# Optimization experiments

Measured on AMD Instinct MI355X. Metric: run time of the kernel, lower is better.

The kernel has to match this reference:

```python
import jax, jax.numpy as jnp
import numpy as np

D = 1024
H = 16
DH = D // H
L = 128  # max_pos_len
B = 4
T = 1024
SCALE = float(np.sqrt(D / H))


def setup_inputs() -> dict:
    key = jax.random.key(0)
    ks = jax.random.split(key, 9)
    x_q = jax.random.normal(ks[0], (B, T, D), dtype=jnp.float32)
    x_k = jax.random.normal(ks[1], (B, T, D), dtype=jnp.float32)
    x_v = jax.random.normal(ks[2], (B, T, D), dtype=jnp.float32)
    mask = jax.random.randint(ks[3], (B, 1, 1, T), 0, 2) == 1  # bool, True = masked
    Wq = jax.random.normal(ks[4], (D, D), dtype=jnp.float32) * 0.02
    Wk = jax.random.normal(ks[5], (D, D), dtype=jnp.float32) * 0.02
    Wv = jax.random.normal(ks[6], (D, D), dtype=jnp.float32) * 0.02
    Wo = jax.random.normal(ks[7], (D, D), dtype=jnp.float32) * 0.02
    pos_emb = jax.random.normal(ks[8], (2 * L + 1, DH), dtype=jnp.float32)
    return {"x_q": x_q, "x_k": x_k, "x_v": x_v, "mask": mask,
            "Wq": Wq, "Wk": Wk, "Wv": Wv, "Wo": Wo, "pos_emb": pos_emb}


def reference(x_q, x_k, x_v, mask, Wq, Wk, Wv, Wo, pos_emb):
    # nn.Linear(bias=False): y = x @ W.T
    def split_heads(x):  # (B,T,D) -> (B,H,T,DH)
        return x.reshape(B, -1, H, DH).transpose(0, 2, 1, 3)

    Q = split_heads(x_q @ Wq.T)
    K = split_heads(x_k @ Wk.T)
    V = split_heads(x_v @ Wv.T)

    logits = jnp.einsum('bhqd,bhkd->bhqk', Q, K)

    # arrange_char_pos_embedding: indices[q,k] = clamp(k-q, -L, L) + L
    rel = jnp.clip(jnp.arange(T)[None, :] - jnp.arange(T)[:, None], -L, L) + L
    arranged_pos = pos_emb[rel]  # (T_Q, T_K, DH)
    pos_logits = jnp.einsum('bhqd,qkd->bhqk', Q, arranged_pos)

    logits = (logits + pos_logits) / SCALE
    logits = jnp.where(mask, -jnp.inf, logits)  # mask broadcasts (B,1,1,T)
    attn = jax.nn.softmax(logits, axis=-1)  # dropout p=0.0 -> identity

    combined = jnp.einsum('bhqk,bhkd->bhqd', attn, V)
    heads_concat = combined.transpose(0, 2, 1, 3).reshape(B, -1, D)
    return heads_concat @ Wo.T
```

## Files before the change

kernel.cpp:

```cpp
#include <hip/hip_runtime.h>
#include <hip/hip_bf16.h>
#include <stdint.h>

typedef __attribute__((ext_vector_type(8))) short short8;
typedef __attribute__((ext_vector_type(4))) float f32x4;

__device__ __forceinline__ uint16_t f2bf(float f) {
    union { float f; uint32_t u; } v; v.f = f;
    uint32_t r = v.u + 0x7FFF + ((v.u >> 16) & 1);
    return (uint16_t)(r >> 16);
}
__device__ __forceinline__ float bf2f(uint16_t u) {
    union { uint32_t u; float f; } v; v.u = ((uint32_t)u) << 16;
    return v.f;
}
__device__ __forceinline__ float exp2_raw(float x) {
    float r;
    asm("v_exp_f32 %0, %1" : "=v"(r) : "v"(x));
    return r;
}
__device__ __forceinline__ uint32_t cvt_pk_bf16(float lo, float hi) {
    uint32_t r;
    asm("v_cvt_pk_bf16_f32 %0, %1, %2" : "=v"(r) : "v"(lo), "v"(hi));
    return r;
}

template<int F32>
__device__ __forceinline__ uint4 load8(const void* p, size_t off) {
    if (F32) {
        const float* f = (const float*)p + off;
        float4 f0 = *(const float4*)f;
        float4 f1 = *(const float4*)(f + 4);
        uint4 r;
        r.x = (uint32_t)f2bf(f0.x) | ((uint32_t)f2bf(f0.y) << 16);
        r.y = (uint32_t)f2bf(f0.z) | ((uint32_t)f2bf(f0.w) << 16);
        r.z = (uint32_t)f2bf(f1.x) | ((uint32_t)f2bf(f1.y) << 16);
        r.w = (uint32_t)f2bf(f1.z) | ((uint32_t)f2bf(f1.w) << 16);
        return r;
    } else {
        return *(const uint4*)((const uint16_t*)p + off);
    }
}

#define GLDS(gp, lp) __builtin_amdgcn_global_load_lds( \
    (const __attribute__((address_space(1))) void*)(gp), \
    (__attribute__((address_space(3))) void*)(lp), 16, 0, 0)

struct CvtSeg { const float* s; uint16_t* d; int n8; };
struct CvtArgs { CvtSeg seg[9]; int nseg; const void* mraw; unsigned long long* mbits; };

__global__ __launch_bounds__(256) void cvt_bf16(CvtArgs a)
{
    if (blockIdx.x == 0) {
        __shared__ int flags[3];
        __shared__ uint8_t mloc[4096];
        const uint32_t* w = (const uint32_t*)a.mraw;
        const uint8_t* b8 = (const uint8_t*)a.mraw;
        const int t = threadIdx.x;
        if (t < 3) flags[t] = 0;
        __syncthreads();
        int fbyte = 0, ff32 = 0, fodd = 0;
        for (int i = t; i < 1024; i += 256) {
            uint32_t v = w[i];
            if (v != 0u && v != 1u && v != 0x3F800000u) fbyte = 1;
            if (v == 0x3F800000u) ff32 = 1;
            if ((i & 1) && v != 0u) fodd = 1;
        }
        if (fbyte) atomicOr(&flags[0], 1);
        if (ff32)  atomicOr(&flags[1], 1);
        if (fodd)  atomicOr(&flags[2], 1);
        __syncthreads();
        int mode;
        if (flags[0]) mode = 1;
        else if (flags[1]) mode = 0;
        else if (!flags[2]) mode = 2;
        else mode = 0;
        for (int k = t; k < 4096; k += 256) {
            int val;
            if (mode == 1)      val = (b8[k] != 0);
            else if (mode == 2) val = (w[2 * k] != 0u);
            else                val = (w[k] != 0u);
            mloc[k] = (uint8_t)val;
        }
        __syncthreads();
        if (t < 64) {
            uint64_t bits = 0;
#pragma unroll
            for (int i = 0; i < 64; ++i)
                bits |= (uint64_t)mloc[t * 64 + i] << i;
            a.mbits[t] = bits;
        }
    }
    const int tid = blockIdx.x * 256 + threadIdx.x;
    const int stride = gridDim.x * 256;
    for (int s = 0; s < a.nseg; ++s) {
        const float* src = a.seg[s].s;
        uint16_t* dst = a.seg[s].d;
        const int n8 = a.seg[s].n8;
        if (src) {
            for (int i = tid; i < n8; i += stride)
                *(uint4*)(dst + (size_t)i * 8) = load8<1>(src, (size_t)i * 8);
        } else {
            const uint4 z = {0u, 0u, 0u, 0u};
            for (int i = tid; i < n8; i += stride)
                *(uint4*)(dst + (size_t)i * 8) = z;
        }
    }
}

__global__ __launch_bounds__(256) void gemm128_qkv(
    const uint16_t* __restrict__ xq, const uint16_t* __restrict__ xk, const uint16_t* __restrict__ xv,
    const uint16_t* __restrict__ Wq, const uint16_t* __restrict__ Wk, const uint16_t* __restrict__ Wv,
    uint16_t* __restrict__ Qh, uint16_t* __restrict__ Khd, uint16_t* __restrict__ Vt)
{
    __shared__ alignas(16) uint16_t As[2][128 * 32];
    __shared__ alignas(16) uint16_t Bs[2][128 * 32];

    const int z = blockIdx.z;
    const uint16_t* A = (z == 0) ? xq : (z == 1) ? xk : xv;
    const uint16_t* B = (z == 0) ? Wq : (z == 1) ? Wk : Wv;
    uint16_t* C = (z == 0) ? Qh : (z == 1) ? Khd : Vt;
    const int cm = (z == 2) ? 2 : 1;
    const int bm = blockIdx.x, bn = blockIdx.y;
    const int K = 1024;

    const int t = threadIdx.x;
    const int lane = t & 63, wave = t >> 6;
    const int lrow = lane & 15, quad = lane >> 4;
    const int wr = (wave >> 1) * 64, wc = (wave & 1) * 64;
    const int g_row = wave * 16 + (lane >> 2);
    const int g_col = (lane & 3) * 8;

    const f32x4 fz = {0.f, 0.f, 0.f, 0.f};
    f32x4 acc[4][4];
#pragma unroll
    for (int i = 0; i < 4; ++i)
#pragma unroll
        for (int j = 0; j < 4; ++j) acc[i][j] = fz;

    for (int k0 = 0; k0 < K; k0 += 64) {
        __syncthreads();
#pragma unroll
        for (int kh = 0; kh < 2; ++kh) {
            const int kk = k0 + kh * 32;
            GLDS(A + (size_t)(bm * 128 + g_row) * K + kk + g_col,      As[kh] + wave * 512);
            GLDS(A + (size_t)(bm * 128 + g_row + 64) * K + kk + g_col, As[kh] + wave * 512 + 2048);
            GLDS(B + (size_t)(bn * 128 + g_row) * K + kk + g_col,      Bs[kh] + wave * 512);
            GLDS(B + (size_t)(bn * 128 + g_row + 64) * K + kk + g_col, Bs[kh] + wave * 512 + 2048);
        }
        __syncthreads();

#pragma unroll
        for (int kh = 0; kh < 2; ++kh) {
            short8 a[4], b[4];
#pragma unroll
            for (int i = 0; i < 4; ++i)
                a[i] = *(const short8*)(As[kh] + (wr + i * 16 + lrow) * 32 + quad * 8);
#pragma unroll
            for (int j = 0; j < 4; ++j)
                b[j] = *(const short8*)(Bs[kh] + (wc + j * 16 + lrow) * 32 + quad * 8);
#pragma unroll
            for (int i = 0; i < 4; ++i)
#pragma unroll
                for (int j = 0; j < 4; ++j)
                    acc[i][j] = __builtin_amdgcn_mfma_f32_16x16x32_bf16(a[i], b[j], acc[i][j], 0, 0, 0);
        }
    }

    if (cm == 2) {
        __syncthreads();
        uint16_t* scr = As[0] + wave * 1024;
#pragma unroll
        for (int i = 0; i < 4; ++i)
#pragma unroll
            for (int j = 0; j < 4; ++j) {
                uint2 pk;
                pk.x = (uint32_t)f2bf(acc[i][j][0]) | ((uint32_t)f2bf(acc[i][j][1]) << 16);
                pk.y = (uint32_t)f2bf(acc[i][j][2]) | ((uint32_t)f2bf(acc[i][j][3]) << 16);
                *(uint2*)(scr + lrow * 16 + quad * 4) = pk;
                if (lane < 32) {
                    int n = lane >> 1, m8 = (lane & 1) * 8;
                    short8 vv = *(const short8*)(scr + n * 16 + m8);
                    int ng = bn * 128 + wc + j * 16 + n;
                    int hh = ng >> 6, d = ng & 63;
                    int mg = bm * 128 + wr + i * 16;
                    int bb = mg >> 10, tl = (mg & 1023) + m8;
                    *(short8*)(C + ((((size_t)bb * 16 + hh) * 64 + d) * 1024 + tl)) = vv;
                }
            }
        return;
    }

#pragma unroll
    for (int i = 0; i < 4; ++i)
#pragma unroll
        for (int j = 0; j < 4; ++j)
#pragma unroll
            for (int r = 0; r < 4; ++r) {
                int m = bm * 128 + wr + i * 16 + quad * 4 + r;
                int n = bn * 128 + wc + j * 16 + lrow;
                int bb = m >> 10, tt = m & 1023, hh = n >> 6, d = n & 63;
                C[(((size_t)bb * 16 + hh) * 1024 + tt) * 64 + d] = f2bf(acc[i][j][r]);
            }
}

__global__ __launch_bounds__(256) void gemm_out(
    const uint16_t* __restrict__ A, const uint16_t* __restrict__ B,
    float* __restrict__ C, int M, int N, int K)
{
    __shared__ alignas(16) uint16_t As[2][64 * 32];
    __shared__ alignas(16) uint16_t Bs[2][128 * 32];

    const int t = threadIdx.x;
    const int lane = t & 63, wave = t >> 6;
    const int lrow = lane & 15, quad = lane >> 4;
    const int wr = (wave >> 1) * 32, wc = (wave & 1) * 64;
    const int g_row = wave * 16 + (lane >> 2);
    const int g_col = (lane & 3) * 8;
    const int bm = blockIdx.x, bn = blockIdx.y;

    const f32x4 fz = {0.f, 0.f, 0.f, 0.f};
    f32x4 acc[2][4];
#pragma unroll
    for (int i = 0; i < 2; ++i)
#pragma unroll
        for (int j = 0; j < 4; ++j) acc[i][j] = fz;

    for (int k0 = 0; k0 < K; k0 += 64) {
        __syncthreads();
#pragma unroll
        for (int kh = 0; kh < 2; ++kh) {
            const int kk = k0 + kh * 32;
            GLDS(A + (size_t)(bm * 64 + g_row) * K + kk + g_col,       As[kh] + wave * 512);
            GLDS(B + (size_t)(bn * 128 + g_row) * K + kk + g_col,      Bs[kh] + wave * 512);
            GLDS(B + (size_t)(bn * 128 + g_row + 64) * K + kk + g_col, Bs[kh] + wave * 512 + 2048);
        }
        __syncthreads();

#pragma unroll
        for (int kh = 0; kh < 2; ++kh) {
            short8 a[2], b[4];
#pragma unroll
            for (int i = 0; i < 2; ++i)
                a[i] = *(const short8*)(As[kh] + (wr + i * 16 + lrow) * 32 + quad * 8);
#pragma unroll
            for (int j = 0; j < 4; ++j)
                b[j] = *(const short8*)(Bs[kh] + (wc + j * 16 + lrow) * 32 + quad * 8);
#pragma unroll
            for (int i = 0; i < 2; ++i)
#pragma unroll
                for (int j = 0; j < 4; ++j)
                    acc[i][j] = __builtin_amdgcn_mfma_f32_16x16x32_bf16(a[i], b[j], acc[i][j], 0, 0, 0);
        }
    }

#pragma unroll
    for (int i = 0; i < 2; ++i)
#pragma unroll
        for (int j = 0; j < 4; ++j)
#pragma unroll
            for (int r = 0; r < 4; ++r) {
                int m = bm * 64 + wr + i * 16 + quad * 4 + r;
                int n = bn * 128 + wc + j * 16 + lrow;
                C[(size_t)m * N + n] = acc[i][j][r];
            }
}

__global__ __launch_bounds__(256) void flash_attn(
    const uint16_t* __restrict__ Qh, const uint16_t* __restrict__ Kh,
    const uint16_t* __restrict__ Vt, const uint16_t* __restrict__ pos,
    const unsigned long long* __restrict__ mask64, uint16_t* __restrict__ comb)
{
    const int blk = blockIdx.x;
    const int jj = blk >> 3;
    const int bh = (blk & 7) * 8 + (jj >> 4);
    const int qt = jj & 15;
    const int b = bh >> 4;
    const int h = bh & 15;
    const int t = threadIdx.x;
    const int lane = t & 63;
    const int wave = t >> 6;
    const int lrow = lane & 15;
    const int quad = lane >> 4;
    const int qb = qt * 64 + wave * 16;

    __shared__ alignas(16) uint16_t Ks[2][4096];
    __shared__ alignas(16) uint16_t Vs[2][4096];
    __shared__ alignas(16) uint16_t Qpos_l[64][277];
    __shared__ alignas(16) uint16_t Pl[4][16][72];

    const uint16_t* Kp = Kh + (size_t)bh * 65536;
    const uint16_t* Vp = Vt + (size_t)bh * 65536;
    const unsigned long long* mk64 = mask64 + b * 16;

    const int sg_r = lane >> 2;
    const int sg_c = ((lane & 3) ^ ((sg_r >> 1) & 3)) * 8;
    const int hw = wave >> 1;
    const int gw = (wave & 1) * 2;
    const int rdc = (quad ^ ((lrow >> 1) & 3)) * 8;

    const float CS = 0.18033688011f;

#pragma unroll
    for (int gg = 0; gg < 2; ++gg) {
        int g = gw + gg;
        GLDS(Kp + (size_t)(g * 16 + sg_r) * 64 + hw * 32 + sg_c, &Ks[0][hw * 2048 + g * 512]);
        GLDS(Vp + (size_t)(g * 16 + sg_r) * 1024 + hw * 32 + sg_c, &Vs[0][hw * 2048 + g * 512]);
    }

    const uint16_t* Qp = Qh + ((size_t)bh * 1024 + qb) * 64;
    short8 aq0 = *(const short8*)(Qp + (size_t)lrow * 64 + quad * 8);
    short8 aq1 = *(const short8*)(Qp + (size_t)lrow * 64 + 32 + quad * 8);

    const f32x4 fz = {0.f, 0.f, 0.f, 0.f};

#pragma unroll 4
    for (int nt = 0; nt < 17; ++nt) {
        short8 pb0 = *(const short8*)(pos + (size_t)(nt * 16 + lrow) * 64 + quad * 8);
        short8 pb1 = *(const short8*)(pos + (size_t)(nt * 16 + lrow) * 64 + 32 + quad * 8);
        f32x4 c = __builtin_amdgcn_mfma_f32_16x16x32_bf16(aq0, pb0, fz, 0, 0, 0);
        c = __builtin_amdgcn_mfma_f32_16x16x32_bf16(aq1, pb1, c, 0, 0, 0);
        const uint32_t p01 = cvt_pk_bf16(c[0] * CS, c[1] * CS);
        const uint32_t p23 = cvt_pk_bf16(c[2] * CS, c[3] * CS);
        const int row = wave * 16 + quad * 4;
        const int col = nt * 16 + lrow;
        Qpos_l[row + 0][col] = (uint16_t)p01;
        Qpos_l[row + 1][col] = (uint16_t)(p01 >> 16);
        Qpos_l[row + 2][col] = (uint16_t)p23;
        Qpos_l[row + 3][col] = (uint16_t)(p23 >> 16);
    }

    float pcl[4], pch[4];
#pragma unroll
    for (int r = 0; r < 4; ++r) {
        int ql = wave * 16 + quad * 4 + r;
        pcl[r] = bf2f(Qpos_l[ql][0]);
        pch[r] = bf2f(Qpos_l[ql][256]);
    }

    f32x4 o[4] = {fz, fz, fz, fz};
    float lsum[4] = {0.f, 0.f, 0.f, 0.f};

    for (int kb = 0; kb < 1024; kb += 64) {
        const int cur = (kb >> 6) & 1;
        __syncthreads();
        if (kb + 64 < 1024) {
            const int nxt = cur ^ 1;
#pragma unroll
            for (int gg = 0; gg < 2; ++gg) {
                int g = gw + gg;
                GLDS(Kp + (size_t)(kb + 64 + g * 16 + sg_r) * 64 + hw * 32 + sg_c,
                     &Ks[nxt][hw * 2048 + g * 512]);
                GLDS(Vp + (size_t)(g * 16 + sg_r) * 1024 + kb + 64 + hw * 32 + sg_c,
                     &Vs[nxt][hw * 2048 + g * 512]);
            }
        }
        const uint16_t* Kc = Ks[cur];
        const uint16_t* Vc = Vs[cur];
        const unsigned long long mb = mk64[kb >> 6];

        f32x4 s[4];
        __builtin_amdgcn_s_setprio(1);
#pragma unroll
        for (int j = 0; j < 4; ++j) {
            short8 k0 = *(const short8*)(Kc + (j * 16 + lrow) * 32 + rdc);
            short8 k1 = *(const short8*)(Kc + 2048 + (j * 16 + lrow) * 32 + rdc);
            s[j] = __builtin_amdgcn_mfma_f32_16x16x32_bf16(aq0, k0, fz, 0, 0, 0);
            s[j] = __builtin_amdgcn_mfma_f32_16x16x32_bf16(aq1, k1, s[j], 0, 0, 0);
        }
        __builtin_amdgcn_s_setprio(0);

        const int diff = kb - qb;
        if (diff <= -192 || diff >= 144) {
            const bool low = (diff <= -192);
#pragma unroll
            for (int j = 0; j < 4; ++j) {
                const uint32_t mj = ((uint32_t)(mb >> (j * 16)) >> lrow) & 1u;
                float e[4];
#pragma unroll
                for (int r = 0; r < 4; ++r) {
                    float pc = low ? pcl[r] : pch[r];
                    float ev = exp2_raw(__builtin_fmaf(s[j][r], CS, pc));
                    ev = mj ? 0.f : ev;
                    lsum[r] += ev;
                    e[r] = ev;
                }
                const uint32_t p01 = cvt_pk_bf16(e[0], e[1]);
                const uint32_t p23 = cvt_pk_bf16(e[2], e[3]);
                const int col = j * 16 + lrow;
                const int rw = quad * 4;
                Pl[wave][rw + 0][col] = (uint16_t)p01;
                Pl[wave][rw + 1][col] = (uint16_t)(p01 >> 16);
                Pl[wave][rw + 2][col] = (uint16_t)p23;
                Pl[wave][rw + 3][col] = (uint16_t)(p23 >> 16);
            }
        } else {
#pragma unroll
            for (int j = 0; j < 4; ++j) {
                const int key = kb + j * 16 + lrow;
                const uint32_t mj = ((uint32_t)(mb >> (j * 16)) >> lrow) & 1u;
                float e[4];
#pragma unroll
                for (int r = 0; r < 4; ++r) {
                    int q = qb + quad * 4 + r;
                    int ql = q & 63;
                    int rel = min(max(key - q, -128), 128) + 128;
                    float p = bf2f(Qpos_l[ql][rel]);
                    float ev = exp2_raw(__builtin_fmaf(s[j][r], CS, p));
                    ev = mj ? 0.f : ev;
                    lsum[r] += ev;
                    e[r] = ev;
                }
                const uint32_t p01 = cvt_pk_bf16(e[0], e[1]);
                const uint32_t p23 = cvt_pk_bf16(e[2], e[3]);
                const int col = j * 16 + lrow;
                const int rw = quad * 4;
                Pl[wave][rw + 0][col] = (uint16_t)p01;
                Pl[wave][rw + 1][col] = (uint16_t)(p01 >> 16);
                Pl[wave][rw + 2][col] = (uint16_t)p23;
                Pl[wave][rw + 3][col] = (uint16_t)(p23 >> 16);
            }
        }
        short8 ap0 = *(const short8*)(&Pl[wave][lrow][quad * 8]);
        short8 ap1 = *(const short8*)(&Pl[wave][lrow][32 + quad * 8]);

        __builtin_amdgcn_s_setprio(1);
#pragma unroll
        for (int dt = 0; dt < 4; ++dt) {
            short8 v0 = *(const short8*)(Vc + (dt * 16 + lrow) * 32 + rdc);
            short8 v1 = *(const short8*)(Vc + 2048 + (dt * 16 + lrow) * 32 + rdc);
            o[dt] = __builtin_amdgcn_mfma_f32_16x16x32_bf16(ap0, v0, o[dt], 0, 0, 0);
            o[dt] = __builtin_amdgcn_mfma_f32_16x16x32_bf16(ap1, v1, o[dt], 0, 0, 0);
        }
        __builtin_amdgcn_s_setprio(0);
    }

#pragma unroll
    for (int off = 1; off < 16; off <<= 1)
#pragma unroll
        for (int r = 0; r < 4; ++r)
            lsum[r] += __shfl_xor(lsum[r], off);

    float inv[4];
#pragma unroll
    for (int r = 0; r < 4; ++r) inv[r] = 1.0f / lsum[r];

#pragma unroll
    for (int dt = 0; dt < 4; ++dt)
#pragma unroll
        for (int r = 0; r < 4; ++r) {
            size_t row = (size_t)b * 1024 + qb + quad * 4 + r;
            size_t col = (size_t)h * 64 + dt * 16 + lrow;
            comb[row * 1024 + col] = f2bf(o[dt][r] * inv[r]);
        }
}

extern "C" void kernel_launch(void* const* d_in, const int* in_sizes, int n_in,
                              void* d_out, int out_size, void* d_ws, size_t ws_size,
                              hipStream_t stream)
{
    const float* x_q = (const float*)d_in[0];
    const float* x_k = (const float*)d_in[1];
    const float* x_v = (const float*)d_in[2];
    const void*  msk = d_in[3];
    const float* Wq  = (const float*)d_in[4];
    const float* Wk  = (const float*)d_in[5];
    const float* Wv  = (const float*)d_in[6];
    const float* Wo  = (const float*)d_in[7];
    const float* pos = (const float*)d_in[8];

    char* ws = (char*)d_ws;
    const size_t MB = 1u << 20;
    uint16_t* Qh   = (uint16_t*)(ws);
    uint16_t* Khd  = (uint16_t*)(ws + 8 * MB);
    uint16_t* Vt   = (uint16_t*)(ws + 16 * MB);
    uint16_t* xqb  = (uint16_t*)(ws + 24 * MB);
    uint16_t* xkb  = (uint16_t*)(ws + 32 * MB);
    uint16_t* xvb  = (uint16_t*)(ws + 40 * MB);
    uint16_t* Wqb  = (uint16_t*)(ws + 48 * MB);
    uint16_t* Wkb  = (uint16_t*)(ws + 50 * MB);
    uint16_t* Wvb  = (uint16_t*)(ws + 52 * MB);
    uint16_t* Wob  = (uint16_t*)(ws + 54 * MB);
    uint16_t* posb = (uint16_t*)(ws + 56 * MB);
    unsigned long long* mbits = (unsigned long long*)(ws + 56 * MB + 65536);
    uint16_t* comb = xqb;

    CvtArgs ca{};
    int ns = 0;
    ca.seg[ns++] = {x_q, xqb, 524288};
    ca.seg[ns++] = {x_k, xkb, 524288};
    ca.seg[ns++] = {x_v, xvb, 524288};
    ca.seg[ns++] = {Wq, Wqb, 131072};
    ca.seg[ns++] = {Wk, Wkb, 131072};
    ca.seg[ns++] = {Wv, Wvb, 131072};
    ca.seg[ns++] = {Wo, Wob, 131072};
    ca.seg[ns++] = {pos, posb, 2056};
    ca.seg[ns++] = {nullptr, posb + 16448, 120};
    ca.nseg = ns;
    ca.mraw = msk;
    ca.mbits = mbits;
    cvt_bf16<<<dim3(512), dim3(256), 0, stream>>>(ca);

    gemm128_qkv<<<dim3(32, 8, 3), dim3(256), 0, stream>>>(
        xqb, xkb, xvb, Wqb, Wkb, Wvb, Qh, Khd, Vt);

    flash_attn<<<dim3(1024), dim3(256), 0, stream>>>(Qh, Khd, Vt, posb, mbits, comb);

    gemm_out<<<dim3(64, 8), dim3(256), 0, stream>>>(
        comb, Wob, (float*)d_out, 4096, 1024, 1024);
}
```

Measured before the change: 230.0 us.

## Load K/V fragments directly from global into registers, drop LDS staging

Removes the shared-memory K/V double buffer and __syncthreads in the flash attention loop. Each wave now loads its K and V MFMA fragments straight from global memory into registers, prefetching the next K tile one step ahead through ping-pong register arrays (the loop is unrolled by two via a macro). Each of the four waves now fetches the full K/V tile itself, raising global/L2 traffic and register pressure in exchange for no block-wide barriers and less LDS use, which may allow more blocks per CU. The conversion kernel's grid is also doubled.

```diff
diff --git a/kernel.cpp b/kernel.cpp
--- a/kernel.cpp
+++ b/kernel.cpp
@@ -264,6 +264,92 @@
                 int n = bn * 128 + wc + j * 16 + lrow;
                 C[(size_t)m * N + n] = acc[i][j][r];
             }
+}
+
+#define FA_BODY(TI, KC, KN)                                                         \
+{                                                                                   \
+    const int kb = (TI) * 64;                                                       \
+    short8 vv[8];                                                                   \
+    _Pragma("unroll")                                                               \
+    for (int dt = 0; dt < 4; ++dt) {                                                \
+        vv[dt * 2 + 0] = *(const short8*)(Vrow + (size_t)dt * 16384 + kb);          \
+        vv[dt * 2 + 1] = *(const short8*)(Vrow + (size_t)dt * 16384 + kb + 32);     \
+    }                                                                               \
+    const int kbn = (((TI) + 1) & 15) * 64;                                         \
+    _Pragma("unroll")                                                               \
+    for (int j = 0; j < 4; ++j) {                                                   \
+        KN[j * 2 + 0] = *(const short8*)(Krow + (size_t)(kbn + j * 16) * 64);       \
+        KN[j * 2 + 1] = *(const short8*)(Krow + (size_t)(kbn + j * 16) * 64 + 32);  \
+    }                                                                               \
+    const unsigned long long mb = mk64[(TI)];                                       \
+    f32x4 s[4];                                                                     \
+    __builtin_amdgcn_s_setprio(1);                                                  \
+    _Pragma("unroll")                                                               \
+    for (int j = 0; j < 4; ++j) {                                                   \
+        s[j] = __builtin_amdgcn_mfma_f32_16x16x32_bf16(aq0, KC[j * 2 + 0], fz, 0, 0, 0); \
+        s[j] = __builtin_amdgcn_mfma_f32_16x16x32_bf16(aq1, KC[j * 2 + 1], s[j], 0, 0, 0); \
+    }                                                                               \
+    __builtin_amdgcn_s_setprio(0);                                                  \
+    const int diff = kb - qb;                                                       \
+    if (diff <= -192 || diff >= 144) {                                              \
+        const bool low = (diff <= -192);                                            \
+        _Pragma("unroll")                                                           \
+        for (int j = 0; j < 4; ++j) {                                               \
+            const uint32_t mj = ((uint32_t)(mb >> (j * 16)) >> lrow) & 1u;          \
+            float e[4];                                                             \
+            _Pragma("unroll")                                                       \
+            for (int r = 0; r < 4; ++r) {                                           \
+                float pc = low ? pcl[r] : pch[r];                                   \
+                float ev = exp2_raw(__builtin_fmaf(s[j][r], CS, pc));               \
+                ev = mj ? 0.f : ev;                                                 \
+                lsum[r] += ev;                                                      \
+                e[r] = ev;                                                          \
+            }                                                                       \
+            const uint32_t p01 = cvt_pk_bf16(e[0], e[1]);                           \
+            const uint32_t p23 = cvt_pk_bf16(e[2], e[3]);                           \
+            const int col = j * 16 + lrow;                                          \
+            const int rw = quad * 4;                                                \
+            Pl[wave][rw + 0][col] = (uint16_t)p01;                                  \
+            Pl[wave][rw + 1][col] = (uint16_t)(p01 >> 16);                          \
+            Pl[wave][rw + 2][col] = (uint16_t)p23;                                  \
+            Pl[wave][rw + 3][col] = (uint16_t)(p23 >> 16);                          \
+        }                                                                           \
+    } else {                                                                        \
+        _Pragma("unroll")                                                           \
+        for (int j = 0; j < 4; ++j) {                                               \
+            const int key = kb + j * 16 + lrow;                                     \
+            const uint32_t mj = ((uint32_t)(mb >> (j * 16)) >> lrow) & 1u;          \
+            float e[4];                                                             \
+            _Pragma("unroll")                                                       \
+            for (int r = 0; r < 4; ++r) {                                           \
+                int q = qb + quad * 4 + r;                                          \
+                int ql = q & 63;                                                    \
+                int rel = min(max(key - q, -128), 128) + 128;                       \
+                float p = bf2f(Qpos_l[ql][rel]);                                    \
+                float ev = exp2_raw(__builtin_fmaf(s[j][r], CS, p));                \
+                ev = mj ? 0.f : ev;                                                 \
+                lsum[r] += ev;                                                      \
+                e[r] = ev;                                                          \
+            }                                                                       \
+            const uint32_t p01 = cvt_pk_bf16(e[0], e[1]);                           \
+            const uint32_t p23 = cvt_pk_bf16(e[2], e[3]);                           \
+            const int col = j * 16 + lrow;                                          \
+            const int rw = quad * 4;                                                \
+            Pl[wave][rw + 0][col] = (uint16_t)p01;                                  \
+            Pl[wave][rw + 1][col] = (uint16_t)(p01 >> 16);                          \
+            Pl[wave][rw + 2][col] = (uint16_t)p23;                                  \
+            Pl[wave][rw + 3][col] = (uint16_t)(p23 >> 16);                          \
+        }                                                                           \
+    }                                                                               \
+    short8 ap0 = *(const short8*)(&Pl[wave][lrow][quad * 8]);                       \
+    short8 ap1 = *(const short8*)(&Pl[wave][lrow][32 + quad * 8]);                  \
+    __builtin_amdgcn_s_setprio(1);                                                  \
+    _Pragma("unroll")                                                               \
+    for (int dt = 0; dt < 4; ++dt) {                                                \
+        o[dt] = __builtin_amdgcn_mfma_f32_16x16x32_bf16(ap0, vv[dt * 2 + 0], o[dt], 0, 0, 0); \
+        o[dt] = __builtin_amdgcn_mfma_f32_16x16x32_bf16(ap1, vv[dt * 2 + 1], o[dt], 0, 0, 0); \
+    }                                                                               \
+    __builtin_amdgcn_s_setprio(0);                                                  \
 }
 
 __global__ __launch_bounds__(256) void flash_attn(
@@ -284,8 +370,6 @@
     const int quad = lane >> 4;
     const int qb = qt * 64 + wave * 16;
 
-    __shared__ alignas(16) uint16_t Ks[2][4096];
-    __shared__ alignas(16) uint16_t Vs[2][4096];
     __shared__ alignas(16) uint16_t Qpos_l[64][277];
     __shared__ alignas(16) uint16_t Pl[4][16][72];
 
@@ -293,26 +377,23 @@
     const uint16_t* Vp = Vt + (size_t)bh * 65536;
     const unsigned long long* mk64 = mask64 + b * 16;
 
-    const int sg_r = lane >> 2;
-    const int sg_c = ((lane & 3) ^ ((sg_r >> 1) & 3)) * 8;
-    const int hw = wave >> 1;
-    const int gw = (wave & 1) * 2;
-    const int rdc = (quad ^ ((lrow >> 1) & 3)) * 8;
-
     const float CS = 0.18033688011f;
 
-#pragma unroll
-    for (int gg = 0; gg < 2; ++gg) {
-        int g = gw + gg;
-        GLDS(Kp + (size_t)(g * 16 + sg_r) * 64 + hw * 32 + sg_c, &Ks[0][hw * 2048 + g * 512]);
-        GLDS(Vp + (size_t)(g * 16 + sg_r) * 1024 + hw * 32 + sg_c, &Vs[0][hw * 2048 + g * 512]);
-    }
+    const uint16_t* Krow = Kp + (size_t)lrow * 64 + quad * 8;
+    const uint16_t* Vrow = Vp + (size_t)lrow * 1024 + quad * 8;
 
     const uint16_t* Qp = Qh + ((size_t)bh * 1024 + qb) * 64;
     short8 aq0 = *(const short8*)(Qp + (size_t)lrow * 64 + quad * 8);
     short8 aq1 = *(const short8*)(Qp + (size_t)lrow * 64 + 32 + quad * 8);
 
     const f32x4 fz = {0.f, 0.f, 0.f, 0.f};
+
+    short8 ka[8], kn[8];
+#pragma unroll
+    for (int j = 0; j < 4; ++j) {
+        ka[j * 2 + 0] = *(const short8*)(Krow + (size_t)(j * 16) * 64);
+        ka[j * 2 + 1] = *(const short8*)(Krow + (size_t)(j * 16) * 64 + 32);
+    }
 
 #pragma unroll 4
     for (int nt = 0; nt < 17; ++nt) {
@@ -341,98 +422,9 @@
     f32x4 o[4] = {fz, fz, fz, fz};
     float lsum[4] = {0.f, 0.f, 0.f, 0.f};
 
-    for (int kb = 0; kb < 1024; kb += 64) {
-        const int cur = (kb >> 6) & 1;
-        __syncthreads();
-        if (kb + 64 < 1024) {
-            const int nxt = cur ^ 1;
-#pragma unroll
-            for (int gg = 0; gg < 2; ++gg) {
-                int g = gw + gg;
-                GLDS(Kp + (size_t)(kb + 64 + g * 16 + sg_r) * 64 + hw * 32 + sg_c,
-                     &Ks[nxt][hw * 2048 + g * 512]);
-                GLDS(Vp + (size_t)(g * 16 + sg_r) * 1024 + kb + 64 + hw * 32 + sg_c,
-                     &Vs[nxt][hw * 2048 + g * 512]);
-            }
-        }
-        const uint16_t* Kc = Ks[cur];
-        const uint16_t* Vc = Vs[cur];
-        const unsigned long long mb = mk64[kb >> 6];
-
-        f32x4 s[4];
-        __builtin_amdgcn_s_setprio(1);
-#pragma unroll
-        for (int j = 0; j < 4; ++j) {
-            short8 k0 = *(const short8*)(Kc + (j * 16 + lrow) * 32 + rdc);
-            short8 k1 = *(const short8*)(Kc + 2048 + (j * 16 + lrow) * 32 + rdc);
-            s[j] = __builtin_amdgcn_mfma_f32_16x16x32_bf16(aq0, k0, fz, 0, 0, 0);
-            s[j] = __builtin_amdgcn_mfma_f32_16x16x32_bf16(aq1, k1, s[j], 0, 0, 0);
-        }
-        __builtin_amdgcn_s_setprio(0);
-
-        const int diff = kb - qb;
-        if (diff <= -192 || diff >= 144) {
-            const bool low = (diff <= -192);
-#pragma unroll
-            for (int j = 0; j < 4; ++j) {
-                const uint32_t mj = ((uint32_t)(mb >> (j * 16)) >> lrow) & 1u;
-                float e[4];
-#pragma unroll
-                for (int r = 0; r < 4; ++r) {
-                    float pc = low ? pcl[r] : pch[r];
-                    float ev = exp2_raw(__builtin_fmaf(s[j][r], CS, pc));
-                    ev = mj ? 0.f : ev;
-                    lsum[r] += ev;
-                    e[r] = ev;
-                }
-                const uint32_t p01 = cvt_pk_bf16(e[0], e[1]);
-                const uint32_t p23 = cvt_pk_bf16(e[2], e[3]);
-                const int col = j * 16 + lrow;
-                const int rw = quad * 4;
-                Pl[wave][rw + 0][col] = (uint16_t)p01;
-                Pl[wave][rw + 1][col] = (uint16_t)(p01 >> 16);
-                Pl[wave][rw + 2][col] = (uint16_t)p23;
-                Pl[wave][rw + 3][col] = (uint16_t)(p23 >> 16);
-            }
-        } else {
-#pragma unroll
-            for (int j = 0; j < 4; ++j) {
-                const int key = kb + j * 16 + lrow;
-                const uint32_t mj = ((uint32_t)(mb >> (j * 16)) >> lrow) & 1u;
-                float e[4];
-#pragma unroll
-                for (int r = 0; r < 4; ++r) {
-                    int q = qb + quad * 4 + r;
-                    int ql = q & 63;
-                    int rel = min(max(key - q, -128), 128) + 128;
-                    float p = bf2f(Qpos_l[ql][rel]);
-                    float ev = exp2_raw(__builtin_fmaf(s[j][r], CS, p));
-                    ev = mj ? 0.f : ev;
-                    lsum[r] += ev;
-                    e[r] = ev;
-                }
-                const uint32_t p01 = cvt_pk_bf16(e[0], e[1]);
-                const uint32_t p23 = cvt_pk_bf16(e[2], e[3]);
-                const int col = j * 16 + lrow;
-                const int rw = quad * 4;
-                Pl[wave][rw + 0][col] = (uint16_t)p01;
-                Pl[wave][rw + 1][col] = (uint16_t)(p01 >> 16);
-                Pl[wave][rw + 2][col] = (uint16_t)p23;
-                Pl[wave][rw + 3][col] = (uint16_t)(p23 >> 16);
-            }
-        }
-        short8 ap0 = *(const short8*)(&Pl[wave][lrow][quad * 8]);
-        short8 ap1 = *(const short8*)(&Pl[wave][lrow][32 + quad * 8]);
-
-        __builtin_amdgcn_s_setprio(1);
-#pragma unroll
-        for (int dt = 0; dt < 4; ++dt) {
-            short8 v0 = *(const short8*)(Vc + (dt * 16 + lrow) * 32 + rdc);
-            short8 v1 = *(const short8*)(Vc + 2048 + (dt * 16 + lrow) * 32 + rdc);
-            o[dt] = __builtin_amdgcn_mfma_f32_16x16x32_bf16(ap0, v0, o[dt], 0, 0, 0);
-            o[dt] = __builtin_amdgcn_mfma_f32_16x16x32_bf16(ap1, v1, o[dt], 0, 0, 0);
-        }
-        __builtin_amdgcn_s_setprio(0);
+    for (int t2 = 0; t2 < 16; t2 += 2) {
+        FA_BODY(t2, ka, kn)
+        FA_BODY(t2 + 1, kn, ka)
     }
 
 #pragma unroll
@@ -499,7 +491,7 @@
     ca.nseg = ns;
     ca.mraw = msk;
     ca.mbits = mbits;
-    cvt_bf16<<<dim3(512), dim3(256), 0, stream>>>(ca);
+    cvt_bf16<<<dim3(1024), dim3(256), 0, stream>>>(ca);
 
     gemm128_qkv<<<dim3(32, 8, 3), dim3(256), 0, stream>>>(
         xqb, xkb, xvb, Wqb, Wkb, Wvb, Qh, Khd, Vt);
```

New measurement: 302.1 us. 1.31x slower.

## Fold key mask into V and compute softmax row sums via MFMA

Applied to the files above, without the earlier changes.

Applies the key mask by zeroing the masked rows of V (in the transposed V store of the QKV GEMM). It also computes the softmax denominator as an extra MFMA of P against a bf16 0/1 mask vector held in shared memory. This removes the per-element mask select, the scalar row-sum accumulation and the cross-lane shuffle reduction from the attention inner loop. In exchange there are two extra MFMAs per key block and a bf16-rounded P in the denominator, which changes precision slightly. Because the maximum is not subtracted, overflow behaviour is unchanged.

```diff
diff --git a/kernel.cpp b/kernel.cpp
--- a/kernel.cpp
+++ b/kernel.cpp
@@ -47,7 +47,10 @@
     (__attribute__((address_space(3))) void*)(lp), 16, 0, 0)
 
 struct CvtSeg { const float* s; uint16_t* d; int n8; };
-struct CvtArgs { CvtSeg seg[9]; int nseg; const void* mraw; unsigned long long* mbits; };
+struct CvtArgs {
+    CvtSeg seg[9]; int nseg;
+    const void* mraw; unsigned long long* mbits; uint16_t* mvals;
+};
 
 __global__ __launch_bounds__(256) void cvt_bf16(CvtArgs a)
 {
@@ -83,6 +86,8 @@
             mloc[k] = (uint8_t)val;
         }
         __syncthreads();
+        for (int k = t; k < 4096; k += 256)
+            a.mvals[k] = mloc[k] ? (uint16_t)0 : (uint16_t)0x3F80;
         if (t < 64) {
             uint64_t bits = 0;
 #pragma unroll
@@ -111,7 +116,8 @@
 __global__ __launch_bounds__(256) void gemm128_qkv(
     const uint16_t* __restrict__ xq, const uint16_t* __restrict__ xk, const uint16_t* __restrict__ xv,
     const uint16_t* __restrict__ Wq, const uint16_t* __restrict__ Wk, const uint16_t* __restrict__ Wv,
-    uint16_t* __restrict__ Qh, uint16_t* __restrict__ Khd, uint16_t* __restrict__ Vt)
+    uint16_t* __restrict__ Qh, uint16_t* __restrict__ Khd, uint16_t* __restrict__ Vt,
+    const unsigned long long* __restrict__ mbits)
 {
     __shared__ alignas(16) uint16_t As[2][128 * 32];
     __shared__ alignas(16) uint16_t Bs[2][128 * 32];
@@ -185,6 +191,18 @@
                     int hh = ng >> 6, d = ng & 63;
                     int mg = bm * 128 + wr + i * 16;
                     int bb = mg >> 10, tl = (mg & 1023) + m8;
+                    uint32_t eb = (uint32_t)(mbits[(size_t)bb * 16 + (tl >> 6)] >> (tl & 63)) & 0xFFu;
+                    if (eb) {
+                        union { short8 s; uint32_t u[4]; } uw;
+                        uw.s = vv;
+#pragma unroll
+                        for (int c = 0; c < 4; ++c) {
+                            uint32_t km = (((eb >> (2 * c)) & 1) ? 0u : 0x0000FFFFu)
+                                        | (((eb >> (2 * c + 1)) & 1) ? 0u : 0xFFFF0000u);
+                            uw.u[c] &= km;
+                        }
+                        vv = uw.s;
+                    }
                     *(short8*)(C + ((((size_t)bb * 16 + hh) * 64 + d) * 1024 + tl)) = vv;
                 }
             }
@@ -269,7 +287,7 @@
 __global__ __launch_bounds__(256) void flash_attn(
     const uint16_t* __restrict__ Qh, const uint16_t* __restrict__ Kh,
     const uint16_t* __restrict__ Vt, const uint16_t* __restrict__ pos,
-    const unsigned long long* __restrict__ mask64, uint16_t* __restrict__ comb)
+    const uint16_t* __restrict__ maskv, uint16_t* __restrict__ comb)
 {
     const int blk = blockIdx.x;
     const int jj = blk >> 3;
@@ -288,10 +306,10 @@
     __shared__ alignas(16) uint16_t Vs[2][4096];
     __shared__ alignas(16) uint16_t Qpos_l[64][277];
     __shared__ alignas(16) uint16_t Pl[4][16][72];
+    __shared__ alignas(16) uint16_t maskl[1024];
 
     const uint16_t* Kp = Kh + (size_t)bh * 65536;
     const uint16_t* Vp = Vt + (size_t)bh * 65536;
-    const unsigned long long* mk64 = mask64 + b * 16;
 
     const int sg_r = lane >> 2;
     const int sg_c = ((lane & 3) ^ ((sg_r >> 1) & 3)) * 8;
@@ -307,6 +325,8 @@
         GLDS(Kp + (size_t)(g * 16 + sg_r) * 64 + hw * 32 + sg_c, &Ks[0][hw * 2048 + g * 512]);
         GLDS(Vp + (size_t)(g * 16 + sg_r) * 1024 + hw * 32 + sg_c, &Vs[0][hw * 2048 + g * 512]);
     }
+    if (wave < 2)
+        GLDS(maskv + (size_t)b * 1024 + wave * 512 + lane * 8, maskl + wave * 512);
 
     const uint16_t* Qp = Qh + ((size_t)bh * 1024 + qb) * 64;
     short8 aq0 = *(const short8*)(Qp + (size_t)lrow * 64 + quad * 8);
@@ -339,7 +359,7 @@
     }
 
     f32x4 o[4] = {fz, fz, fz, fz};
-    float lsum[4] = {0.f, 0.f, 0.f, 0.f};
+    f32x4 lacc = fz;
 
     for (int kb = 0; kb < 1024; kb += 64) {
         const int cur = (kb >> 6) & 1;
@@ -357,7 +377,6 @@
         }
         const uint16_t* Kc = Ks[cur];
         const uint16_t* Vc = Vs[cur];
-        const unsigned long long mb = mk64[kb >> 6];
 
         f32x4 s[4];
         __builtin_amdgcn_s_setprio(1);
@@ -375,15 +394,11 @@
             const bool low = (diff <= -192);
 #pragma unroll
             for (int j = 0; j < 4; ++j) {
-                const uint32_t mj = ((uint32_t)(mb >> (j * 16)) >> lrow) & 1u;
                 float e[4];
 #pragma unroll
                 for (int r = 0; r < 4; ++r) {
                     float pc = low ? pcl[r] : pch[r];
-                    float ev = exp2_raw(__builtin_fmaf(s[j][r], CS, pc));
-                    ev = mj ? 0.f : ev;
-                    lsum[r] += ev;
-                    e[r] = ev;
+                    e[r] = exp2_raw(__builtin_fmaf(s[j][r], CS, pc));
                 }
                 const uint32_t p01 = cvt_pk_bf16(e[0], e[1]);
                 const uint32_t p23 = cvt_pk_bf16(e[2], e[3]);
@@ -398,7 +413,6 @@
 #pragma unroll
             for (int j = 0; j < 4; ++j) {
                 const int key = kb + j * 16 + lrow;
-                const uint32_t mj = ((uint32_t)(mb >> (j * 16)) >> lrow) & 1u;
                 float e[4];
 #pragma unroll
                 for (int r = 0; r < 4; ++r) {
@@ -406,10 +420,7 @@
                     int ql = q & 63;
                     int rel = min(max(key - q, -128), 128) + 128;
                     float p = bf2f(Qpos_l[ql][rel]);
-                    float ev = exp2_raw(__builtin_fmaf(s[j][r], CS, p));
-                    ev = mj ? 0.f : ev;
-                    lsum[r] += ev;
-                    e[r] = ev;
+                    e[r] = exp2_raw(__builtin_fmaf(s[j][r], CS, p));
                 }
                 const uint32_t p01 = cvt_pk_bf16(e[0], e[1]);
                 const uint32_t p23 = cvt_pk_bf16(e[2], e[3]);
@@ -423,6 +434,8 @@
         }
         short8 ap0 = *(const short8*)(&Pl[wave][lrow][quad * 8]);
         short8 ap1 = *(const short8*)(&Pl[wave][lrow][32 + quad * 8]);
+        short8 bm0 = *(const short8*)(maskl + kb + quad * 8);
+        short8 bm1 = *(const short8*)(maskl + kb + 32 + quad * 8);
 
         __builtin_amdgcn_s_setprio(1);
 #pragma unroll
@@ -432,18 +445,14 @@
             o[dt] = __builtin_amdgcn_mfma_f32_16x16x32_bf16(ap0, v0, o[dt], 0, 0, 0);
             o[dt] = __builtin_amdgcn_mfma_f32_16x16x32_bf16(ap1, v1, o[dt], 0, 0, 0);
         }
+        lacc = __builtin_amdgcn_mfma_f32_16x16x32_bf16(ap0, bm0, lacc, 0, 0, 0);
+        lacc = __builtin_amdgcn_mfma_f32_16x16x32_bf16(ap1, bm1, lacc, 0, 0, 0);
         __builtin_amdgcn_s_setprio(0);
     }
 
-#pragma unroll
-    for (int off = 1; off < 16; off <<= 1)
-#pragma unroll
-        for (int r = 0; r < 4; ++r)
-            lsum[r] += __shfl_xor(lsum[r], off);
-
     float inv[4];
 #pragma unroll
-    for (int r = 0; r < 4; ++r) inv[r] = 1.0f / lsum[r];
+    for (int r = 0; r < 4; ++r) inv[r] = 1.0f / lacc[r];
 
 #pragma unroll
     for (int dt = 0; dt < 4; ++dt)
@@ -483,6 +492,7 @@
     uint16_t* Wob  = (uint16_t*)(ws + 54 * MB);
     uint16_t* posb = (uint16_t*)(ws + 56 * MB);
     unsigned long long* mbits = (unsigned long long*)(ws + 56 * MB + 65536);
+    uint16_t* mvals = (uint16_t*)(ws + 56 * MB + 65536 + 4096);
     uint16_t* comb = xqb;
 
     CvtArgs ca{};
@@ -499,12 +509,13 @@
     ca.nseg = ns;
     ca.mraw = msk;
     ca.mbits = mbits;
+    ca.mvals = mvals;
     cvt_bf16<<<dim3(512), dim3(256), 0, stream>>>(ca);
 
     gemm128_qkv<<<dim3(32, 8, 3), dim3(256), 0, stream>>>(
-        xqb, xkb, xvb, Wqb, Wkb, Wvb, Qh, Khd, Vt);
-
-    flash_attn<<<dim3(1024), dim3(256), 0, stream>>>(Qh, Khd, Vt, posb, mbits, comb);
+        xqb, xkb, xvb, Wqb, Wkb, Wvb, Qh, Khd, Vt, mbits);
+
+    flash_attn<<<dim3(1024), dim3(256), 0, stream>>>(Qh, Khd, Vt, posb, mvals, comb);
 
     gemm_out<<<dim3(64, 8), dim3(256), 0, stream>>>(
         comb, Wob, (float*)d_out, 4096, 1024, 1024);
```

New measurement: 237.3 us. 1.03x slower.
